# Kernel optimization log

Hardware: AMD Instinct MI355X
Metric: run time of the kernel (lower is better)

Reference implementation:

```python
import jax, jax.numpy as jnp
import numpy as np
import math


def setup_inputs() -> dict:
    key = jax.random.key(0)
    k1, k2, k3 = jax.random.split(key, 3)
    B, L, H, E = 2, 2048, 8, 64
    queries = jax.random.normal(k1, (B, L, H, E), dtype=jnp.float32)
    keys = jax.random.normal(k2, (B, L, H, E), dtype=jnp.float32)
    values = jax.random.normal(k3, (B, L, H, E), dtype=jnp.float32)
    return {"queries": queries, "keys": keys, "values": values}


def reference(queries, keys, values):
    B, L, H, E = queries.shape
    scale = 1.0 / math.sqrt(E)
    # [B,H,L,S] attention scores
    scores = jnp.einsum('blhe,bshe->bhls', queries, keys)
    # causal mask: positions s > l masked to -inf (scale * -inf stays -inf)
    causal = jnp.triu(jnp.ones((L, L), dtype=bool), k=1)  # True above diagonal
    scores = jnp.where(causal[None, None, :, :], -jnp.inf, scores)
    attn = scale * scores
    SA = jax.nn.softmax(attn, axis=-1)  # dropout p=0.0 -> identity
    V = jnp.einsum('bhls,bshd->blhd', SA, values)
    return (V, SA)
```

## Files before the change

kernel.cpp:

```cpp
#include <hip/hip_runtime.h>
#include <math.h>

#define L_DIM 2048
#define H_DIM 8
#define ROWSTRIDE 512
#define NT 512
#define QSCALE 0.18033688011112042f
#define FLT_BIG 3.402823466e+38f

typedef __attribute__((ext_vector_type(8))) short short8;
typedef __attribute__((ext_vector_type(4))) float floatx4;

__device__ __forceinline__ float fexp2(float x) {
#if __has_builtin(__builtin_amdgcn_exp2f)
    return __builtin_amdgcn_exp2f(x);
#else
    return exp2f(x);
#endif
}

__device__ __forceinline__ float flog2(float x) {
#if __has_builtin(__builtin_amdgcn_logf)
    return __builtin_amdgcn_logf(x);
#else
    return log2f(x);
#endif
}

__device__ __forceinline__ unsigned int cvtpk(float lo, float hi) {
    unsigned int r;
    asm("v_cvt_pk_bf16_f32 %0, %1, %2" : "=v"(r) : "v"(lo), "v"(hi));
    return r;
}

__device__ __forceinline__ short8 pack8(float4 a, float4 b) {
    union { unsigned int u[4]; short8 v; } pk;
    pk.u[0] = cvtpk(a.x, a.y); pk.u[1] = cvtpk(a.z, a.w);
    pk.u[2] = cvtpk(b.x, b.y); pk.u[3] = cvtpk(b.z, b.w);
    return pk.v;
}

__device__ __forceinline__ short8 pack8q(float4 a, float4 b) {
    union { unsigned int u[4]; short8 v; } pk;
    pk.u[0] = cvtpk(a.x * QSCALE, a.y * QSCALE);
    pk.u[1] = cvtpk(a.z * QSCALE, a.w * QSCALE);
    pk.u[2] = cvtpk(b.x * QSCALE, b.y * QSCALE);
    pk.u[3] = cvtpk(b.z * QSCALE, b.w * QSCALE);
    return pk.v;
}

__device__ __forceinline__ int swz(int row, int col) {
    return (row << 6) + ((((col >> 3) ^ (row & 7)) << 3) | (col & 7));
}

__global__ __launch_bounds__(NT, 4)
void attn_mfma7(const float* __restrict__ Q, const float* __restrict__ K,
                const float* __restrict__ Vv, float* __restrict__ outV,
                float* __restrict__ outSA)
{
    __shared__ __align__(16) unsigned char smem[74752];
    unsigned short* Ks = (unsigned short*)(smem);
    unsigned short* Vt = (unsigned short*)(smem + 32768);
    unsigned short* Ps = (unsigned short*)(smem + 65536);
    float* Ml = (float*)(smem + 73728);
    float* Ll = (float*)(smem + 74240);
    float* Ob = (float*)(smem);

    const int t    = threadIdx.x;
    const int lane = t & 63;
    const int w    = t >> 6;
    const int g    = w >> 2;
    const int wg   = w & 3;
    const int l15  = lane & 15;
    const int quad = lane >> 4;
    const int gc   = g << 5;

    const int bid = blockIdx.x;
    const int h   = bid & 7;
    const int b   = (bid >> 3) & 1;
    const int k   = bid >> 4;
    const int qm  = (k < 16) ? k : (47 - k);
    const int qt  = b ? (31 - qm) : qm;
    const int q0  = qt << 6;
    const int ntiles = qt + 1;
    const int nphase = (ntiles + 1) >> 1;

    const float* Qb = Q  + (size_t)b * L_DIM * ROWSTRIDE + h * 64;
    const float* Kb = K  + (size_t)b * L_DIM * ROWSTRIDE + h * 64;
    const float* Vb = Vv + (size_t)b * L_DIM * ROWSTRIDE + h * 64;
    float* saBase = outSA + (size_t)(b * H_DIM + h) * L_DIM * L_DIM;

    const int sr = t >> 3, sc = (t & 7) << 3;
    const int kq = sr & 31;
    const int kpr = (sr & 32) | ((kq & 1) << 4) | (kq >> 1);
    const int kswz = swz(kpr, sc);

    const int rp = t >> 4, ec = (t & 15) << 2;
    const int vswz0 = swz(ec + 0, 2 * rp);
    const int vswz1 = swz(ec + 1, 2 * rp);
    const int vswz2 = swz(ec + 2, 2 * rp);
    const int vswz3 = swz(ec + 3, 2 * rp);

    auto stageK = [&](int bufi, float4 f0, float4 f1) {
        *(short8*)&Ks[(bufi << 12) + kswz] = pack8(f0, f1);
    };
    auto stageV = [&](int bufi, float4 a, float4 bb) {
        unsigned short* Vn = Vt + (bufi << 12);
        *(unsigned int*)&Vn[vswz0] = cvtpk(a.x, bb.x);
        *(unsigned int*)&Vn[vswz1] = cvtpk(a.y, bb.y);
        *(unsigned int*)&Vn[vswz2] = cvtpk(a.z, bb.z);
        *(unsigned int*)&Vn[vswz3] = cvtpk(a.w, bb.w);
    };

    short8 aQ0, aQ1;
    {
        const float* qsrc = Qb + (size_t)(q0 + 16 * wg + l15) * ROWSTRIDE + quad * 8;
        aQ0 = pack8q(*(const float4*)(qsrc),      *(const float4*)(qsrc + 4));
        aQ1 = pack8q(*(const float4*)(qsrc + 32), *(const float4*)(qsrc + 36));
    }

    float m_r[4], l_r[4];
#pragma unroll
    for (int r = 0; r < 4; ++r) { m_r[r] = -FLT_BIG; l_r[r] = 0.f; }

    auto compute1 = [&](int bufi, int st) {
        const unsigned short* Kc = Ks + (bufi << 12);
        floatx4 d0, d1;
        {
            short8 b0 = *(const short8*)&Kc[swz(gc + l15, quad * 8)];
            short8 b1 = *(const short8*)&Kc[swz(gc + l15, 32 + quad * 8)];
            floatx4 acc = {0.f, 0.f, 0.f, 0.f};
            acc = __builtin_amdgcn_mfma_f32_16x16x32_bf16(aQ0, b0, acc, 0, 0, 0);
            acc = __builtin_amdgcn_mfma_f32_16x16x32_bf16(aQ1, b1, acc, 0, 0, 0);
            d0 = acc;
        }
        {
            short8 b0 = *(const short8*)&Kc[swz(gc + 16 + l15, quad * 8)];
            short8 b1 = *(const short8*)&Kc[swz(gc + 16 + l15, 32 + quad * 8)];
            floatx4 acc = {0.f, 0.f, 0.f, 0.f};
            acc = __builtin_amdgcn_mfma_f32_16x16x32_bf16(aQ0, b0, acc, 0, 0, 0);
            acc = __builtin_amdgcn_mfma_f32_16x16x32_bf16(aQ1, b1, acc, 0, 0, 0);
            d1 = acc;
        }
        if (st == qt) {
            const int scol = (st << 6) + gc + 2 * l15;
#pragma unroll
            for (int r = 0; r < 4; ++r) {
                const int lrow = q0 + 16 * wg + quad * 4 + r;
                float v0 = (scol     <= lrow) ? d0[r] : -INFINITY;
                float v1 = (scol + 1 <= lrow) ? d1[r] : -INFINITY;
                const float mnew = fmaxf(m_r[r], fmaxf(v0, v1));
                float es = fexp2(v0 - mnew) + fexp2(v1 - mnew);
                l_r[r] = l_r[r] * fexp2(m_r[r] - mnew) + es;
                m_r[r] = mnew;
            }
        } else {
#pragma unroll
            for (int r = 0; r < 4; ++r) {
                float v0 = d0[r], v1 = d1[r];
                const float mnew = fmaxf(m_r[r], fmaxf(v0, v1));
                float es = fexp2(v0 - mnew) + fexp2(v1 - mnew);
                l_r[r] = l_r[r] * fexp2(m_r[r] - mnew) + es;
                m_r[r] = mnew;
            }
        }
    };

    {
        const int t1 = (ntiles > 1) ? 1 : 0;
        const float* k0 = Kb + (size_t)sr * ROWSTRIDE + sc;
        const float* k1 = Kb + (size_t)((t1 << 6) + sr) * ROWSTRIDE + sc;
        stageK(0, *(const float4*)k0, *(const float4*)(k0 + 4));
        stageK(1, *(const float4*)k1, *(const float4*)(k1 + 4));
    }
    __syncthreads();

    for (int ph = 0; ph < nphase; ++ph) {
        const int base = ph << 1;
        const int pb   = (ph & 1) << 1;
        const int t2 = (base + 2 < ntiles) ? base + 2 : ntiles - 1;
        const int t3 = (base + 3 < ntiles) ? base + 3 : ntiles - 1;
        const float* k2 = Kb + (size_t)((t2 << 6) + sr) * ROWSTRIDE + sc;
        const float* k3 = Kb + (size_t)((t3 << 6) + sr) * ROWSTRIDE + sc;
        float4 a2 = *(const float4*)k2, b2 = *(const float4*)(k2 + 4);
        float4 a3 = *(const float4*)k3, b3 = *(const float4*)(k3 + 4);

        compute1(pb, base);
        if (base + 1 < ntiles) compute1(pb + 1, base + 1);

        if (base + 2 < ntiles) stageK(pb ^ 2, a2, b2);
        if (base + 3 < ntiles) stageK((pb ^ 2) + 1, a3, b3);
        __syncthreads();
    }

#pragma unroll
    for (int r = 0; r < 4; ++r) {
#pragma unroll
        for (int mk = 1; mk < 16; mk <<= 1) {
            float mo = __shfl_xor(m_r[r], mk);
            float lo = __shfl_xor(l_r[r], mk);
            float mn = fmaxf(m_r[r], mo);
            l_r[r] = l_r[r] * fexp2(m_r[r] - mn) + lo * fexp2(mo - mn);
            m_r[r] = mn;
        }
    }

    if (l15 == 0) {
#pragma unroll
        for (int r = 0; r < 4; ++r) {
            const int row = 16 * wg + quad * 4 + r;
            Ml[g * 64 + row] = m_r[r];
            Ll[g * 64 + row] = l_r[r];
        }
    }
    {
        const int t1 = (ntiles > 1) ? 1 : 0;
        const float* k0 = Kb + (size_t)sr * ROWSTRIDE + sc;
        const float* k1 = Kb + (size_t)((t1 << 6) + sr) * ROWSTRIDE + sc;
        stageK(0, *(const float4*)k0, *(const float4*)(k0 + 4));
        stageK(1, *(const float4*)k1, *(const float4*)(k1 + 4));
        const float* v0p = Vb + (size_t)(2 * rp) * ROWSTRIDE + ec;
        const float* v1p = Vb + (size_t)((t1 << 6) + 2 * rp) * ROWSTRIDE + ec;
        stageV(0, *(const float4*)v0p, *(const float4*)(v0p + ROWSTRIDE));
        stageV(1, *(const float4*)v1p, *(const float4*)(v1p + ROWSTRIDE));
    }
    __syncthreads();

    float c_r[4];
#pragma unroll
    for (int r = 0; r < 4; ++r) {
        const int row = 16 * wg + quad * 4 + r;
        float m0 = Ml[row], m1 = Ml[64 + row];
        float l0 = Ll[row], l1 = Ll[64 + row];
        float mf = fmaxf(m0, m1);
        float lf = l0 * fexp2(m0 - mf) + l1 * fexp2(m1 - mf);
        c_r[r] = mf + flog2(lf);
    }

    floatx4 oacc[4];
#pragma unroll
    for (int j = 0; j < 4; ++j) oacc[j] = (floatx4){0.f, 0.f, 0.f, 0.f};

    auto compute2 = [&](int bufi, int st) {
        const unsigned short* Kc = Ks + (bufi << 12);
        const unsigned short* Vc = Vt + (bufi << 12);
        floatx4 d0, d1;
        {
            short8 b0 = *(const short8*)&Kc[swz(gc + l15, quad * 8)];
            short8 b1 = *(const short8*)&Kc[swz(gc + l15, 32 + quad * 8)];
            floatx4 acc = {0.f, 0.f, 0.f, 0.f};
            acc = __builtin_amdgcn_mfma_f32_16x16x32_bf16(aQ0, b0, acc, 0, 0, 0);
            acc = __builtin_amdgcn_mfma_f32_16x16x32_bf16(aQ1, b1, acc, 0, 0, 0);
            d0 = acc;
        }
        {
            short8 b0 = *(const short8*)&Kc[swz(gc + 16 + l15, quad * 8)];
            short8 b1 = *(const short8*)&Kc[swz(gc + 16 + l15, 32 + quad * 8)];
            floatx4 acc = {0.f, 0.f, 0.f, 0.f};
            acc = __builtin_amdgcn_mfma_f32_16x16x32_bf16(aQ0, b0, acc, 0, 0, 0);
            acc = __builtin_amdgcn_mfma_f32_16x16x32_bf16(aQ1, b1, acc, 0, 0, 0);
            d1 = acc;
        }
        const int s0 = st << 6;
        const int scol = s0 + gc + 2 * l15;
        if (st == qt) {
#pragma unroll
            for (int r = 0; r < 4; ++r) {
                const int lrow = q0 + 16 * wg + quad * 4 + r;
                const float cr = c_r[r];
                float p0 = (scol     <= lrow) ? fexp2(d0[r] - cr) : 0.0f;
                float p1 = (scol + 1 <= lrow) ? fexp2(d1[r] - cr) : 0.0f;
                float2 pr; pr.x = p0; pr.y = p1;
                *(float2*)(saBase + (size_t)lrow * L_DIM + scol) = pr;
                *(unsigned int*)&Ps[swz(16 * wg + quad * 4 + r, gc + 2 * l15)] = cvtpk(p0, p1);
            }
        } else {
#pragma unroll
            for (int r = 0; r < 4; ++r) {
                const int lrow = q0 + 16 * wg + quad * 4 + r;
                const float cr = c_r[r];
                float p0 = fexp2(d0[r] - cr);
                float p1 = fexp2(d1[r] - cr);
                float2 pr; pr.x = p0; pr.y = p1;
                *(float2*)(saBase + (size_t)lrow * L_DIM + scol) = pr;
                *(unsigned int*)&Ps[swz(16 * wg + quad * 4 + r, gc + 2 * l15)] = cvtpk(p0, p1);
            }
        }
        short8 aP = *(const short8*)&Ps[swz(16 * wg + l15, gc + quad * 8)];
#pragma unroll
        for (int j = 0; j < 4; ++j) {
            short8 bv = *(const short8*)&Vc[swz(16 * j + l15, gc + quad * 8)];
            oacc[j] = __builtin_amdgcn_mfma_f32_16x16x32_bf16(aP, bv, oacc[j], 0, 0, 0);
        }
    };

    for (int ph = 0; ph < nphase; ++ph) {
        const int base = ph << 1;
        const int pb   = (ph & 1) << 1;
        const int t2 = (base + 2 < ntiles) ? base + 2 : ntiles - 1;
        const int t3 = (base + 3 < ntiles) ? base + 3 : ntiles - 1;
        const float* k2 = Kb + (size_t)((t2 << 6) + sr) * ROWSTRIDE + sc;
        const float* k3 = Kb + (size_t)((t3 << 6) + sr) * ROWSTRIDE + sc;
        const float* v2 = Vb + (size_t)((t2 << 6) + 2 * rp) * ROWSTRIDE + ec;
        const float* v3 = Vb + (size_t)((t3 << 6) + 2 * rp) * ROWSTRIDE + ec;
        float4 ka2 = *(const float4*)k2, kb2 = *(const float4*)(k2 + 4);
        float4 ka3 = *(const float4*)k3, kb3 = *(const float4*)(k3 + 4);
        float4 va2 = *(const float4*)v2, vb2 = *(const float4*)(v2 + ROWSTRIDE);
        float4 va3 = *(const float4*)v3, vb3 = *(const float4*)(v3 + ROWSTRIDE);

        compute2(pb, base);
        if (base + 1 < ntiles) compute2(pb + 1, base + 1);

        if (base + 2 < ntiles) { stageK(pb ^ 2, ka2, kb2); stageV(pb ^ 2, va2, vb2); }
        if (base + 3 < ntiles) { stageK((pb ^ 2) + 1, ka3, kb3); stageV((pb ^ 2) + 1, va3, vb3); }
        __syncthreads();
    }

    if (g == 1) {
#pragma unroll
        for (int r = 0; r < 4; ++r) {
            const int row = 16 * wg + quad * 4 + r;
#pragma unroll
            for (int j = 0; j < 4; ++j)
                Ob[row * 65 + 16 * j + l15] = oacc[j][r];
        }
    }
    __syncthreads();
    if (g == 0) {
#pragma unroll
        for (int r = 0; r < 4; ++r) {
            const int row = 16 * wg + quad * 4 + r;
            float* op = outV + ((size_t)b * L_DIM + q0 + row) * ROWSTRIDE + h * 64 + l15;
#pragma unroll
            for (int j = 0; j < 4; ++j)
                op[16 * j] = oacc[j][r] + Ob[row * 65 + 16 * j + l15];
        }
    }

    {
        const int z0 = ntiles << 6;
        const int zr = t >> 3;
        float* rowp = saBase + (size_t)(q0 + zr) * L_DIM;
        const float4 zf = {0.f, 0.f, 0.f, 0.f};
        for (int s = z0 + (t & 7) * 4; s < L_DIM; s += 32)
            *(float4*)(rowp + s) = zf;
    }
}

extern "C" void kernel_launch(void* const* d_in, const int* in_sizes, int n_in,
                              void* d_out, int out_size, void* d_ws, size_t ws_size,
                              hipStream_t stream) {
    const float* Q  = (const float*)d_in[0];
    const float* K  = (const float*)d_in[1];
    const float* Vv = (const float*)d_in[2];
    float* out   = (float*)d_out;
    float* outV  = out;
    float* outSA = out + (size_t)2 * L_DIM * H_DIM * 64;

    dim3 grid(512);
    dim3 block(NT);
    attn_mfma7<<<grid, block, 0, stream>>>(Q, K, Vv, outV, outSA);
}
```

Baseline: 328.9 us.

## Split softmax statistics into separate LSE kernel without running max

Moves the first-pass row-sum computation into its own 256-thread kernel that writes log-sum-exp to workspace, and the PV kernel reads it instead of recomputing statistics in-block. The LSE pass drops the running-max rescaling and sums exp2 of raw scores directly. Barriers are replaced with a custom lgkmcnt wait plus s_barrier. This risks overflow for large scores and adds a second launch plus a workspace round trip.

```diff
diff --git a/kernel.cpp b/kernel.cpp
--- a/kernel.cpp
+++ b/kernel.cpp
@@ -4,9 +4,7 @@
 #define L_DIM 2048
 #define H_DIM 8
 #define ROWSTRIDE 512
-#define NT 512
 #define QSCALE 0.18033688011112042f
-#define FLT_BIG 3.402823466e+38f
 
 typedef __attribute__((ext_vector_type(8))) short short8;
 typedef __attribute__((ext_vector_type(4))) float floatx4;
@@ -53,17 +51,114 @@
     return (row << 6) + ((((col >> 3) ^ (row & 7)) << 3) | (col & 7));
 }
 
-__global__ __launch_bounds__(NT, 4)
-void attn_mfma7(const float* __restrict__ Q, const float* __restrict__ K,
-                const float* __restrict__ Vv, float* __restrict__ outV,
-                float* __restrict__ outSA)
+__device__ __forceinline__ void sbar() {
+    asm volatile("s_waitcnt lgkmcnt(0)" ::: "memory");
+    __builtin_amdgcn_s_barrier();
+    asm volatile("" ::: "memory");
+}
+
+#define DECODE_BLOCK()                                            \
+    const int bid = blockIdx.x;                                   \
+    const int h   = bid & 7;                                      \
+    const int b   = (bid >> 3) & 1;                               \
+    const int kk  = bid >> 4;                                     \
+    const int qm  = (kk < 16) ? kk : (47 - kk);                   \
+    const int qt  = b ? (31 - qm) : qm;                           \
+    const int q0  = qt << 6;                                      \
+    const int ntiles = qt + 1;
+
+__global__ __launch_bounds__(256, 4)
+void attn_lse9(const float* __restrict__ Q, const float* __restrict__ K,
+               float* __restrict__ lse)
 {
-    __shared__ __align__(16) unsigned char smem[74752];
+    __shared__ __align__(16) unsigned short Ks[2][4096];
+
+    const int t    = threadIdx.x;
+    const int lane = t & 63;
+    const int w    = t >> 6;
+    const int l15  = lane & 15;
+    const int quad = lane >> 4;
+
+    DECODE_BLOCK();
+
+    const float* Qb = Q + (size_t)b * L_DIM * ROWSTRIDE + h * 64;
+    const float* Kb = K + (size_t)b * L_DIM * ROWSTRIDE + h * 64;
+    float* lout = lse + (size_t)(b * H_DIM + h) * L_DIM;
+
+    const int sr = t >> 2, sc = (t & 3) << 4;
+    const int ksz0 = swz(sr, sc), ksz1 = swz(sr, sc + 8);
+
+    short8 aQ0, aQ1;
+    {
+        const float* qsrc = Qb + (size_t)(q0 + 16 * w + l15) * ROWSTRIDE + quad * 8;
+        aQ0 = pack8q(*(const float4*)(qsrc),      *(const float4*)(qsrc + 4));
+        aQ1 = pack8q(*(const float4*)(qsrc + 32), *(const float4*)(qsrc + 36));
+    }
+
+    float l_r[4] = {0.f, 0.f, 0.f, 0.f};
+
+    {
+        const float* src = Kb + (size_t)sr * ROWSTRIDE + sc;
+        *(short8*)&Ks[0][ksz0] = pack8(*(const float4*)(src),     *(const float4*)(src + 4));
+        *(short8*)&Ks[0][ksz1] = pack8(*(const float4*)(src + 8), *(const float4*)(src + 12));
+    }
+    sbar();
+
+    for (int st = 0; st < ntiles; ++st) {
+        const int cur = st & 1;
+        const int stp = (st + 1 < ntiles) ? (st + 1) : st;
+        const float* ksrc = Kb + (size_t)((stp << 6) + sr) * ROWSTRIDE + sc;
+        float4 f0 = *(const float4*)(ksrc);
+        float4 f1 = *(const float4*)(ksrc + 4);
+        float4 f2 = *(const float4*)(ksrc + 8);
+        float4 f3 = *(const float4*)(ksrc + 12);
+
+#pragma unroll
+        for (int jj = 0; jj < 4; ++jj) {
+            short8 b0 = *(const short8*)&Ks[cur][swz(16 * jj + l15, quad * 8)];
+            short8 b1 = *(const short8*)&Ks[cur][swz(16 * jj + l15, 32 + quad * 8)];
+            floatx4 z = {0.f, 0.f, 0.f, 0.f};
+            floatx4 d = __builtin_amdgcn_mfma_f32_16x16x32_bf16(aQ1, b1,
+                        __builtin_amdgcn_mfma_f32_16x16x32_bf16(aQ0, b0, z, 0, 0, 0), 0, 0, 0);
+            if (st == qt) {
+                const int scol = (st << 6) + 16 * jj + l15;
+#pragma unroll
+                for (int r = 0; r < 4; ++r)
+                    l_r[r] += (scol <= q0 + 16 * w + quad * 4 + r) ? fexp2(d[r]) : 0.f;
+            } else {
+#pragma unroll
+                for (int r = 0; r < 4; ++r) l_r[r] += fexp2(d[r]);
+            }
+        }
+
+        if (st + 1 < ntiles) {
+            *(short8*)&Ks[cur ^ 1][ksz0] = pack8(f0, f1);
+            *(short8*)&Ks[cur ^ 1][ksz1] = pack8(f2, f3);
+        }
+        sbar();
+    }
+
+#pragma unroll
+    for (int r = 0; r < 4; ++r) {
+#pragma unroll
+        for (int mk = 1; mk < 16; mk <<= 1) l_r[r] += __shfl_xor(l_r[r], mk);
+    }
+    if (l15 == 0) {
+#pragma unroll
+        for (int r = 0; r < 4; ++r)
+            lout[q0 + 16 * w + quad * 4 + r] = flog2(l_r[r]);
+    }
+}
+
+__global__ __launch_bounds__(512, 4)
+void attn_pv9(const float* __restrict__ Q, const float* __restrict__ K,
+              const float* __restrict__ Vv, float* __restrict__ outV,
+              float* __restrict__ outSA, const float* __restrict__ lse)
+{
+    __shared__ __align__(16) unsigned char smem[73728];
     unsigned short* Ks = (unsigned short*)(smem);
     unsigned short* Vt = (unsigned short*)(smem + 32768);
     unsigned short* Ps = (unsigned short*)(smem + 65536);
-    float* Ml = (float*)(smem + 73728);
-    float* Ll = (float*)(smem + 74240);
     float* Ob = (float*)(smem);
 
     const int t    = threadIdx.x;
@@ -75,20 +170,20 @@
     const int quad = lane >> 4;
     const int gc   = g << 5;
 
-    const int bid = blockIdx.x;
-    const int h   = bid & 7;
-    const int b   = (bid >> 3) & 1;
-    const int k   = bid >> 4;
-    const int qm  = (k < 16) ? k : (47 - k);
-    const int qt  = b ? (31 - qm) : qm;
-    const int q0  = qt << 6;
-    const int ntiles = qt + 1;
+    DECODE_BLOCK();
     const int nphase = (ntiles + 1) >> 1;
 
     const float* Qb = Q  + (size_t)b * L_DIM * ROWSTRIDE + h * 64;
     const float* Kb = K  + (size_t)b * L_DIM * ROWSTRIDE + h * 64;
     const float* Vb = Vv + (size_t)b * L_DIM * ROWSTRIDE + h * 64;
     float* saBase = outSA + (size_t)(b * H_DIM + h) * L_DIM * L_DIM;
+
+    float c_r[4];
+    {
+        const float4 cv = *(const float4*)(lse + (size_t)(b * H_DIM + h) * L_DIM
+                                           + q0 + 16 * wg + quad * 4);
+        c_r[0] = cv.x; c_r[1] = cv.y; c_r[2] = cv.z; c_r[3] = cv.w;
+    }
 
     const int sr = t >> 3, sc = (t & 7) << 3;
     const int kq = sr & 31;
@@ -117,124 +212,6 @@
         const float* qsrc = Qb + (size_t)(q0 + 16 * wg + l15) * ROWSTRIDE + quad * 8;
         aQ0 = pack8q(*(const float4*)(qsrc),      *(const float4*)(qsrc + 4));
         aQ1 = pack8q(*(const float4*)(qsrc + 32), *(const float4*)(qsrc + 36));
-    }
-
-    float m_r[4], l_r[4];
-#pragma unroll
-    for (int r = 0; r < 4; ++r) { m_r[r] = -FLT_BIG; l_r[r] = 0.f; }
-
-    auto compute1 = [&](int bufi, int st) {
-        const unsigned short* Kc = Ks + (bufi << 12);
-        floatx4 d0, d1;
-        {
-            short8 b0 = *(const short8*)&Kc[swz(gc + l15, quad * 8)];
-            short8 b1 = *(const short8*)&Kc[swz(gc + l15, 32 + quad * 8)];
-            floatx4 acc = {0.f, 0.f, 0.f, 0.f};
-            acc = __builtin_amdgcn_mfma_f32_16x16x32_bf16(aQ0, b0, acc, 0, 0, 0);
-            acc = __builtin_amdgcn_mfma_f32_16x16x32_bf16(aQ1, b1, acc, 0, 0, 0);
-            d0 = acc;
-        }
-        {
-            short8 b0 = *(const short8*)&Kc[swz(gc + 16 + l15, quad * 8)];
-            short8 b1 = *(const short8*)&Kc[swz(gc + 16 + l15, 32 + quad * 8)];
-            floatx4 acc = {0.f, 0.f, 0.f, 0.f};
-            acc = __builtin_amdgcn_mfma_f32_16x16x32_bf16(aQ0, b0, acc, 0, 0, 0);
-            acc = __builtin_amdgcn_mfma_f32_16x16x32_bf16(aQ1, b1, acc, 0, 0, 0);
-            d1 = acc;
-        }
-        if (st == qt) {
-            const int scol = (st << 6) + gc + 2 * l15;
-#pragma unroll
-            for (int r = 0; r < 4; ++r) {
-                const int lrow = q0 + 16 * wg + quad * 4 + r;
-                float v0 = (scol     <= lrow) ? d0[r] : -INFINITY;
-                float v1 = (scol + 1 <= lrow) ? d1[r] : -INFINITY;
-                const float mnew = fmaxf(m_r[r], fmaxf(v0, v1));
-                float es = fexp2(v0 - mnew) + fexp2(v1 - mnew);
-                l_r[r] = l_r[r] * fexp2(m_r[r] - mnew) + es;
-                m_r[r] = mnew;
-            }
-        } else {
-#pragma unroll
-            for (int r = 0; r < 4; ++r) {
-                float v0 = d0[r], v1 = d1[r];
-                const float mnew = fmaxf(m_r[r], fmaxf(v0, v1));
-                float es = fexp2(v0 - mnew) + fexp2(v1 - mnew);
-                l_r[r] = l_r[r] * fexp2(m_r[r] - mnew) + es;
-                m_r[r] = mnew;
-            }
-        }
-    };
-
-    {
-        const int t1 = (ntiles > 1) ? 1 : 0;
-        const float* k0 = Kb + (size_t)sr * ROWSTRIDE + sc;
-        const float* k1 = Kb + (size_t)((t1 << 6) + sr) * ROWSTRIDE + sc;
-        stageK(0, *(const float4*)k0, *(const float4*)(k0 + 4));
-        stageK(1, *(const float4*)k1, *(const float4*)(k1 + 4));
-    }
-    __syncthreads();
-
-    for (int ph = 0; ph < nphase; ++ph) {
-        const int base = ph << 1;
-        const int pb   = (ph & 1) << 1;
-        const int t2 = (base + 2 < ntiles) ? base + 2 : ntiles - 1;
-        const int t3 = (base + 3 < ntiles) ? base + 3 : ntiles - 1;
-        const float* k2 = Kb + (size_t)((t2 << 6) + sr) * ROWSTRIDE + sc;
-        const float* k3 = Kb + (size_t)((t3 << 6) + sr) * ROWSTRIDE + sc;
-        float4 a2 = *(const float4*)k2, b2 = *(const float4*)(k2 + 4);
-        float4 a3 = *(const float4*)k3, b3 = *(const float4*)(k3 + 4);
-
-        compute1(pb, base);
-        if (base + 1 < ntiles) compute1(pb + 1, base + 1);
-
-        if (base + 2 < ntiles) stageK(pb ^ 2, a2, b2);
-        if (base + 3 < ntiles) stageK((pb ^ 2) + 1, a3, b3);
-        __syncthreads();
-    }
-
-#pragma unroll
-    for (int r = 0; r < 4; ++r) {
-#pragma unroll
-        for (int mk = 1; mk < 16; mk <<= 1) {
-            float mo = __shfl_xor(m_r[r], mk);
-            float lo = __shfl_xor(l_r[r], mk);
-            float mn = fmaxf(m_r[r], mo);
-            l_r[r] = l_r[r] * fexp2(m_r[r] - mn) + lo * fexp2(mo - mn);
-            m_r[r] = mn;
-        }
-    }
-
-    if (l15 == 0) {
-#pragma unroll
-        for (int r = 0; r < 4; ++r) {
-            const int row = 16 * wg + quad * 4 + r;
-            Ml[g * 64 + row] = m_r[r];
-            Ll[g * 64 + row] = l_r[r];
-        }
-    }
-    {
-        const int t1 = (ntiles > 1) ? 1 : 0;
-        const float* k0 = Kb + (size_t)sr * ROWSTRIDE + sc;
-        const float* k1 = Kb + (size_t)((t1 << 6) + sr) * ROWSTRIDE + sc;
-        stageK(0, *(const float4*)k0, *(const float4*)(k0 + 4));
-        stageK(1, *(const float4*)k1, *(const float4*)(k1 + 4));
-        const float* v0p = Vb + (size_t)(2 * rp) * ROWSTRIDE + ec;
-        const float* v1p = Vb + (size_t)((t1 << 6) + 2 * rp) * ROWSTRIDE + ec;
-        stageV(0, *(const float4*)v0p, *(const float4*)(v0p + ROWSTRIDE));
-        stageV(1, *(const float4*)v1p, *(const float4*)(v1p + ROWSTRIDE));
-    }
-    __syncthreads();
-
-    float c_r[4];
-#pragma unroll
-    for (int r = 0; r < 4; ++r) {
-        const int row = 16 * wg + quad * 4 + r;
-        float m0 = Ml[row], m1 = Ml[64 + row];
-        float l0 = Ll[row], l1 = Ll[64 + row];
-        float mf = fmaxf(m0, m1);
-        float lf = l0 * fexp2(m0 - mf) + l1 * fexp2(m1 - mf);
-        c_r[r] = mf + flog2(lf);
     }
 
     floatx4 oacc[4];
@@ -293,6 +270,19 @@
             oacc[j] = __builtin_amdgcn_mfma_f32_16x16x32_bf16(aP, bv, oacc[j], 0, 0, 0);
         }
     };
+
+    {
+        const int t1 = (ntiles > 1) ? 1 : 0;
+        const float* k0 = Kb + (size_t)sr * ROWSTRIDE + sc;
+        const float* k1 = Kb + (size_t)((t1 << 6) + sr) * ROWSTRIDE + sc;
+        stageK(0, *(const float4*)k0, *(const float4*)(k0 + 4));
+        stageK(1, *(const float4*)k1, *(const float4*)(k1 + 4));
+        const float* v0p = Vb + (size_t)(2 * rp) * ROWSTRIDE + ec;
+        const float* v1p = Vb + (size_t)((t1 << 6) + 2 * rp) * ROWSTRIDE + ec;
+        stageV(0, *(const float4*)v0p, *(const float4*)(v0p + ROWSTRIDE));
+        stageV(1, *(const float4*)v1p, *(const float4*)(v1p + ROWSTRIDE));
+    }
+    sbar();
 
     for (int ph = 0; ph < nphase; ++ph) {
         const int base = ph << 1;
@@ -313,7 +303,7 @@
 
         if (base + 2 < ntiles) { stageK(pb ^ 2, ka2, kb2); stageV(pb ^ 2, va2, vb2); }
         if (base + 3 < ntiles) { stageK((pb ^ 2) + 1, ka3, kb3); stageV((pb ^ 2) + 1, va3, vb3); }
-        __syncthreads();
+        sbar();
     }
 
     if (g == 1) {
@@ -325,7 +315,7 @@
                 Ob[row * 65 + 16 * j + l15] = oacc[j][r];
         }
     }
-    __syncthreads();
+    sbar();
     if (g == 0) {
 #pragma unroll
         for (int r = 0; r < 4; ++r) {
@@ -356,8 +346,8 @@
     float* out   = (float*)d_out;
     float* outV  = out;
     float* outSA = out + (size_t)2 * L_DIM * H_DIM * 64;
-
-    dim3 grid(512);
-    dim3 block(NT);
-    attn_mfma7<<<grid, block, 0, stream>>>(Q, K, Vv, outV, outSA);
-}
+    float* lse   = (float*)d_ws;
+
+    attn_lse9<<<dim3(512), dim3(256), 0, stream>>>(Q, K, lse);
+    attn_pv9<<<dim3(512), dim3(512), 0, stream>>>(Q, K, Vv, outV, outSA, lse);
+}
```

After: 354.6 us. 7.8% more time.

## Interleave causal-mask zero stores into compute loops with balanced tile remapping

Applied to the files above, without the earlier changes.

Zeroing of the masked SA region is reassigned so each block zeroes the tail of the complementary query tile (31-qt), balancing per-block work against the causal compute length. The zero stores are spread across both main loop phases so global writes overlap with MFMA compute instead of trailing at the end. __syncthreads is replaced by a barrier that waits only on LDS counters, avoiding draining outstanding global stores. This relies on the compiler still inserting correct vmcnt waits for global loads feeding LDS staging.

```diff
diff --git a/kernel.cpp b/kernel.cpp
--- a/kernel.cpp
+++ b/kernel.cpp
@@ -53,10 +53,16 @@
     return (row << 6) + ((((col >> 3) ^ (row & 7)) << 3) | (col & 7));
 }
 
+__device__ __forceinline__ void sbar() {
+    asm volatile("s_waitcnt lgkmcnt(0)" ::: "memory");
+    __builtin_amdgcn_s_barrier();
+    asm volatile("" ::: "memory");
+}
+
 __global__ __launch_bounds__(NT, 4)
-void attn_mfma7(const float* __restrict__ Q, const float* __restrict__ K,
-                const float* __restrict__ Vv, float* __restrict__ outV,
-                float* __restrict__ outSA)
+void attn_mfma10(const float* __restrict__ Q, const float* __restrict__ K,
+                 const float* __restrict__ Vv, float* __restrict__ outV,
+                 float* __restrict__ outSA)
 {
     __shared__ __align__(16) unsigned char smem[74752];
     unsigned short* Ks = (unsigned short*)(smem);
@@ -78,8 +84,8 @@
     const int bid = blockIdx.x;
     const int h   = bid & 7;
     const int b   = (bid >> 3) & 1;
-    const int k   = bid >> 4;
-    const int qm  = (k < 16) ? k : (47 - k);
+    const int kk  = bid >> 4;
+    const int qm  = (kk < 16) ? kk : (47 - kk);
     const int qt  = b ? (31 - qm) : qm;
     const int q0  = qt << 6;
     const int ntiles = qt + 1;
@@ -89,6 +95,13 @@
     const float* Kb = K  + (size_t)b * L_DIM * ROWSTRIDE + h * 64;
     const float* Vb = Vv + (size_t)b * L_DIM * ROWSTRIDE + h * 64;
     float* saBase = outSA + (size_t)(b * H_DIM + h) * L_DIM * L_DIM;
+
+    const int Tz = 31 - qt;
+    const int zn = 2 * qt;
+    int zj = 0;
+    float* zb = saBase + (size_t)(64 * Tz + (t >> 3)) * L_DIM + 64 * (Tz + 1)
+                + ((t & 7) << 2);
+    const float4 zf4 = {0.f, 0.f, 0.f, 0.f};
 
     const int sr = t >> 3, sc = (t & 7) << 3;
     const int kq = sr & 31;
@@ -110,6 +123,12 @@
         *(unsigned int*)&Vn[vswz1] = cvtpk(a.y, bb.y);
         *(unsigned int*)&Vn[vswz2] = cvtpk(a.z, bb.z);
         *(unsigned int*)&Vn[vswz3] = cvtpk(a.w, bb.w);
+    };
+    auto zslice = [&]() {
+        if (zj < zn) {
+            *(float4*)(zb + (zj << 5)) = zf4; ++zj;
+            if (zj < zn) { *(float4*)(zb + (zj << 5)) = zf4; ++zj; }
+        }
     };
 
     short8 aQ0, aQ1;
@@ -173,7 +192,7 @@
         stageK(0, *(const float4*)k0, *(const float4*)(k0 + 4));
         stageK(1, *(const float4*)k1, *(const float4*)(k1 + 4));
     }
-    __syncthreads();
+    sbar();
 
     for (int ph = 0; ph < nphase; ++ph) {
         const int base = ph << 1;
@@ -188,9 +207,11 @@
         compute1(pb, base);
         if (base + 1 < ntiles) compute1(pb + 1, base + 1);
 
+        zslice();
+
         if (base + 2 < ntiles) stageK(pb ^ 2, a2, b2);
         if (base + 3 < ntiles) stageK((pb ^ 2) + 1, a3, b3);
-        __syncthreads();
+        sbar();
     }
 
 #pragma unroll
@@ -224,7 +245,7 @@
         stageV(0, *(const float4*)v0p, *(const float4*)(v0p + ROWSTRIDE));
         stageV(1, *(const float4*)v1p, *(const float4*)(v1p + ROWSTRIDE));
     }
-    __syncthreads();
+    sbar();
 
     float c_r[4];
 #pragma unroll
@@ -311,10 +332,14 @@
         compute2(pb, base);
         if (base + 1 < ntiles) compute2(pb + 1, base + 1);
 
+        zslice();
+
         if (base + 2 < ntiles) { stageK(pb ^ 2, ka2, kb2); stageV(pb ^ 2, va2, vb2); }
         if (base + 3 < ntiles) { stageK((pb ^ 2) + 1, ka3, kb3); stageV((pb ^ 2) + 1, va3, vb3); }
-        __syncthreads();
-    }
+        sbar();
+    }
+
+    while (zj < zn) { *(float4*)(zb + (zj << 5)) = zf4; ++zj; }
 
     if (g == 1) {
 #pragma unroll
@@ -325,7 +350,7 @@
                 Ob[row * 65 + 16 * j + l15] = oacc[j][r];
         }
     }
-    __syncthreads();
+    sbar();
     if (g == 0) {
 #pragma unroll
         for (int r = 0; r < 4; ++r) {
@@ -335,15 +360,6 @@
             for (int j = 0; j < 4; ++j)
                 op[16 * j] = oacc[j][r] + Ob[row * 65 + 16 * j + l15];
         }
-    }
-
-    {
-        const int z0 = ntiles << 6;
-        const int zr = t >> 3;
-        float* rowp = saBase + (size_t)(q0 + zr) * L_DIM;
-        const float4 zf = {0.f, 0.f, 0.f, 0.f};
-        for (int s = z0 + (t & 7) * 4; s < L_DIM; s += 32)
-            *(float4*)(rowp + s) = zf;
     }
 }
 
@@ -359,5 +375,5 @@
 
     dim3 grid(512);
     dim3 block(NT);
-    attn_mfma7<<<grid, block, 0, stream>>>(Q, K, Vv, outV, outSA);
-}
+    attn_mfma10<<<grid, block, 0, stream>>>(Q, K, Vv, outV, outSA);
+}
```

Result: slower. 341.0 us (+3.7%).
